# Performance work log

Hardware: AMD Instinct MI355X
Metric: run time of the kernel (lower is better)

## Reference

```python
import math
import jax, jax.numpy as jnp
import numpy as np

B, L, DIM, H = 2, 2048, 1024, 16
D = DIM // H  # head_dim = 64
EPS = 1e-6


def setup_inputs() -> dict:
    key = jax.random.key(0)
    ks = jax.random.split(key, 5)
    s = 0.02
    return {
        "x": jax.random.normal(ks[0], (B, L, DIM), jnp.float32),
        "pe": jax.random.normal(ks[1], (B, 1, L, D // 2, 2, 2), jnp.float32),
        "w_qkv": jax.random.normal(ks[2], (DIM, 3 * DIM), jnp.float32) * s,
        "q_scale": jnp.ones((D,), jnp.float32),
        "k_scale": jnp.ones((D,), jnp.float32),
        "w_proj": jax.random.normal(ks[3], (DIM, DIM), jnp.float32) * s,
        "b_proj": jnp.zeros((DIM,), jnp.float32),
    }


def _rmsnorm(t, scale):
    # flax nnx.RMSNorm: x * rsqrt(mean(x^2) + eps) * scale, over last dim
    var = jnp.mean(jnp.square(t), axis=-1, keepdims=True)
    return t * jax.lax.rsqrt(var + EPS) * scale


def _apply_rope(t, pe):
    # t: [B,H,L,D]; pe: [B,1,L,D/2,2,2]
    t2 = t.reshape(*t.shape[:-1], D // 2, 1, 2)
    out = pe[..., 0] * t2[..., 0] + pe[..., 1] * t2[..., 1]  # [B,H,L,D/2,2]
    return out.reshape(t.shape)


def reference(x, pe, w_qkv, q_scale, k_scale, w_proj, b_proj):
    # fused QKV projection
    qkv = jnp.einsum('bld,de->ble', x, w_qkv)  # [B,L,3*DIM]
    qkv = qkv.reshape(B, L, 3, H, D).transpose(2, 0, 3, 1, 4)  # [3,B,H,L,D]
    q, k, v = qkv[0], qkv[1], qkv[2]
    # QK RMSNorm
    q = _rmsnorm(q, q_scale)
    k = _rmsnorm(k, k_scale)
    # RoPE via pe
    q = _apply_rope(q, pe)
    k = _apply_rope(k, pe)
    # scaled dot product attention
    scores = jnp.einsum('bhqd,bhkd->bhqk', q, k) / math.sqrt(D)
    attn = jax.nn.softmax(scores, axis=-1)
    o = jnp.einsum('bhqk,bhkd->bhqd', attn, v)  # [B,H,L,D]
    o = o.transpose(0, 2, 1, 3).reshape(B, L, DIM)  # B H L D -> B L (H D)
    # output projection
    return jnp.einsum('bld,de->ble', o, w_proj) + b_proj
```

## Files before the change

### kernel.cpp

```cpp
#include <hip/hip_runtime.h>
#include <math.h>

#define BB 2
#define LL 2048
#define DIMM 1024
#define HH 16
#define DD 64
#define QKV_N 3072

typedef unsigned short u16;
typedef unsigned int u32;
typedef __attribute__((ext_vector_type(8))) short short8;
typedef __attribute__((ext_vector_type(4))) float f32x4;

__device__ __forceinline__ float bf2f(u16 h) {
    unsigned u = ((unsigned)h) << 16;
    return __uint_as_float(u);
}
__device__ __forceinline__ u16 f2bf(float f) {
    unsigned u = __float_as_uint(f);
    u += 0x7fffu + ((u >> 16) & 1u);
    return (u16)(u >> 16);
}
__device__ __forceinline__ u32 pack_bf2(float lo, float hi) {
    u32 a = __float_as_uint(hi) + 0x8000u;
    u32 b = __float_as_uint(lo) + 0x8000u;
    return __builtin_amdgcn_perm(a, b, 0x07060302u);
}
__device__ __forceinline__ void gload16(const u16* g, u16* l) {
    __builtin_amdgcn_global_load_lds(
        (const __attribute__((address_space(1))) void*)g,
        (__attribute__((address_space(3))) void*)l, 16, 0, 0);
}

__global__ __launch_bounds__(256) void convx(
    const float* __restrict__ X, u16* __restrict__ Xb)
{
    int i = (blockIdx.x * 256 + threadIdx.x) * 8;
    float4 a = *(const float4*)&X[i];
    float4 b = *(const float4*)&X[i + 4];
    u16 t[8] = {f2bf(a.x), f2bf(a.y), f2bf(a.z), f2bf(a.w),
                f2bf(b.x), f2bf(b.y), f2bf(b.z), f2bf(b.w)};
    *(uint4*)&Xb[i] = *(uint4*)t;
}

__global__ __launch_bounds__(256) void convt(
    const float* __restrict__ W, u16* __restrict__ Wt, int K, int N)
{
    __shared__ u16 s[64][72];
    const int tid = threadIdx.x;
    const int k0 = blockIdx.x * 64, n0 = blockIdx.y * 64;
#pragma unroll
    for (int t = 0; t < 16; ++t) {
        int flat = t * 256 + tid;
        int kk = flat >> 6, nn = flat & 63;
        s[nn][kk] = f2bf(W[(size_t)(k0 + kk) * N + n0 + nn]);
    }
    __syncthreads();
#pragma unroll
    for (int t = 0; t < 2; ++t) {
        int chunk = t * 256 + tid;
        int nn = chunk >> 3, kc = chunk & 7;
        *(uint4*)&Wt[(size_t)(n0 + nn) * K + k0 + kc * 8] = *(uint4*)&s[nn][kc * 8];
    }
}

__global__ __launch_bounds__(256) void gemm_qkv(
    const u16* __restrict__ A, const u16* __restrict__ Bt,
    u16* __restrict__ C, u16* __restrict__ vt, const float* __restrict__ pe,
    const float* __restrict__ qs, const float* __restrict__ ks)
{
    __shared__ u16 smem[2 * 128 * 64];
    u16* sA = smem;
    u16* sB = smem + 128 * 64;

    const int tid = threadIdx.x;
    const int wave = tid >> 6, lane = tid & 63;
    const int mIdx = lane & 15, quad = lane >> 4;
    const int wr = wave >> 1, wc = wave & 1;
    const int m0 = blockIdx.y * 128, n0 = blockIdx.x * 128;
    const int N = QKV_N, K = DIMM;
    const int lr = lane >> 3, lc = lane & 7;

    f32x4 acc[4][4];
#pragma unroll
    for (int a = 0; a < 4; ++a)
#pragma unroll
        for (int b = 0; b < 4; ++b) acc[a][b] = (f32x4){0.f, 0.f, 0.f, 0.f};

    for (int k0 = 0; k0 < K; k0 += 64) {
#pragma unroll
        for (int j = 0; j < 4; ++j) {
            int r0 = 32 * wave + 8 * j + lr;
            int kc = 8 * (lc ^ (r0 & 7));
            gload16(&A[(size_t)(m0 + r0) * K + k0 + kc], &sA[(32 * wave + 8 * j) * 64]);
            gload16(&Bt[(size_t)(n0 + r0) * K + k0 + kc], &sB[(32 * wave + 8 * j) * 64]);
        }
        __syncthreads();
#pragma unroll
        for (int ks2 = 0; ks2 < 2; ++ks2) {
            short8 af[4], bfr[4];
#pragma unroll
            for (int mt = 0; mt < 4; ++mt) {
                int Ra = 64 * wr + 16 * mt + mIdx;
                af[mt] = *(const short8*)&sA[Ra * 64 + 8 * ((ks2 * 4 + quad) ^ (Ra & 7))];
            }
#pragma unroll
            for (int nt = 0; nt < 4; ++nt) {
                int Rb = 64 * wc + 16 * nt + mIdx;
                bfr[nt] = *(const short8*)&sB[Rb * 64 + 8 * ((ks2 * 4 + quad) ^ (Rb & 7))];
            }
#pragma unroll
            for (int mt = 0; mt < 4; ++mt)
#pragma unroll
                for (int nt = 0; nt < 4; ++nt)
                    acc[mt][nt] = __builtin_amdgcn_mfma_f32_16x16x32_bf16(
                        af[mt], bfr[nt], acc[mt][nt], 0, 0, 0);
        }
        __syncthreads();
    }

    if (n0 >= 2048) {
#pragma unroll
        for (int mt = 0; mt < 4; ++mt) {
            int lofs = 64 * wr + 16 * mt + 4 * quad;
#pragma unroll
            for (int nt = 0; nt < 4; ++nt) {
                int d = 64 * wc + 16 * nt + mIdx;
                uint2 pr;
                pr.x = pack_bf2(acc[mt][nt][0], acc[mt][nt][1]);
                pr.y = pack_bf2(acc[mt][nt][2], acc[mt][nt][3]);
                *(uint2*)&smem[d * 128 + (lofs ^ (8 * (d & 7)))] = pr;
            }
        }
        __syncthreads();
        {
            const int d = tid >> 1, half = tid & 1;
            const int hd = n0 - 2048 + d;
            const int h = hd >> 6, dd = hd & 63;
            const int b = m0 >> 11, l0 = m0 & 2047;
            u16* dst = vt + ((size_t)((b * 16 + h) * 64 + dd)) * LL + l0 + half * 64;
#pragma unroll
            for (int c = 0; c < 8; ++c) {
                int slot = (half * 64 + 8 * c) ^ (8 * (d & 7));
                *(uint4*)&dst[8 * c] = *(const uint4*)&smem[d * 128 + slot];
            }
        }
    } else {
        const float* scv = (n0 < 1024) ? qs : ks;
        const float pre = (n0 < 1024) ? 0.18033688011112042f : 1.0f;
        float scl[4];
#pragma unroll
        for (int nt = 0; nt < 4; ++nt) scl[nt] = scv[16 * nt + mIdx];

#pragma unroll
        for (int mt = 0; mt < 4; ++mt) {
#pragma unroll
            for (int r = 0; r < 4; ++r) {
                float s = 0.f;
#pragma unroll
                for (int nt = 0; nt < 4; ++nt) {
                    float a = acc[mt][nt][r];
                    s += a * a;
                }
                s += __shfl_xor(s, 1);
                s += __shfl_xor(s, 2);
                s += __shfl_xor(s, 4);
                s += __shfl_xor(s, 8);
                float rn = rsqrtf(s * (1.f / 64.f) + 1e-6f);
                int R = m0 + 64 * wr + 16 * mt + quad * 4 + r;
                size_t peo = (size_t)R * 128;
#pragma unroll
                for (int nt = 0; nt < 4; ++nt) {
                    float v = acc[mt][nt][r] * rn * scl[nt];
                    float pp = __shfl_xor(v, 1);
                    float2 pw = *(const float2*)&pe[peo + 2 * (16 * nt + mIdx)];
                    float e  = (mIdx & 1) ? pp : v;
                    float od = (mIdx & 1) ? v : pp;
                    C[(size_t)R * N + n0 + 64 * wc + 16 * nt + mIdx] =
                        f2bf((pw.x * e + pw.y * od) * pre);
                }
            }
        }
    }
}

__global__ __launch_bounds__(256) void gemm_proj(
    const u16* __restrict__ A, const u16* __restrict__ Bt,
    const float* __restrict__ bias, float* __restrict__ C)
{
    __shared__ u16 sA[64 * 64];
    __shared__ u16 sB[128 * 64];

    const int tid = threadIdx.x;
    const int wave = tid >> 6, lane = tid & 63;
    const int mIdx = lane & 15, quad = lane >> 4;
    const int wr = wave >> 1, wc = wave & 1;
    const int m0 = blockIdx.y * 64, n0 = blockIdx.x * 128;
    const int N = DIMM, K = DIMM;
    const int lr = lane >> 3, lc = lane & 7;

    f32x4 acc[2][4];
#pragma unroll
    for (int a = 0; a < 2; ++a)
#pragma unroll
        for (int b = 0; b < 4; ++b) acc[a][b] = (f32x4){0.f, 0.f, 0.f, 0.f};

    for (int k0 = 0; k0 < K; k0 += 64) {
#pragma unroll
        for (int j = 0; j < 2; ++j) {
            int r0 = 16 * wave + 8 * j + lr;
            int kc = 8 * (lc ^ (r0 & 7));
            gload16(&A[(size_t)(m0 + r0) * K + k0 + kc], &sA[(16 * wave + 8 * j) * 64]);
        }
#pragma unroll
        for (int j = 0; j < 4; ++j) {
            int r0 = 32 * wave + 8 * j + lr;
            int kc = 8 * (lc ^ (r0 & 7));
            gload16(&Bt[(size_t)(n0 + r0) * K + k0 + kc], &sB[(32 * wave + 8 * j) * 64]);
        }
        __syncthreads();
#pragma unroll
        for (int ks2 = 0; ks2 < 2; ++ks2) {
            short8 af[2], bfr[4];
#pragma unroll
            for (int mt = 0; mt < 2; ++mt) {
                int Ra = 32 * wr + 16 * mt + mIdx;
                af[mt] = *(const short8*)&sA[Ra * 64 + 8 * ((ks2 * 4 + quad) ^ (Ra & 7))];
            }
#pragma unroll
            for (int nt = 0; nt < 4; ++nt) {
                int Rb = 64 * wc + 16 * nt + mIdx;
                bfr[nt] = *(const short8*)&sB[Rb * 64 + 8 * ((ks2 * 4 + quad) ^ (Rb & 7))];
            }
#pragma unroll
            for (int mt = 0; mt < 2; ++mt)
#pragma unroll
                for (int nt = 0; nt < 4; ++nt)
                    acc[mt][nt] = __builtin_amdgcn_mfma_f32_16x16x32_bf16(
                        af[mt], bfr[nt], acc[mt][nt], 0, 0, 0);
        }
        __syncthreads();
    }

#pragma unroll
    for (int mt = 0; mt < 2; ++mt)
#pragma unroll
        for (int r = 0; r < 4; ++r) {
            int row = m0 + 32 * wr + 16 * mt + quad * 4 + r;
#pragma unroll
            for (int nt = 0; nt < 4; ++nt) {
                int col = n0 + 64 * wc + 16 * nt + mIdx;
                C[(size_t)row * N + col] = acc[mt][nt][r] + bias[col];
            }
        }
}

__global__ __launch_bounds__(256, 2) void attn_mfma(
    const u16* __restrict__ qkv, const u16* __restrict__ vt, u16* __restrict__ o)
{
    __shared__ u16 sK[2][64 * 64];
    __shared__ u16 sVt[2][64 * 64];
    __shared__ u16 sP[128 * 64];

    const int tid = threadIdx.x;
    const int wave = tid >> 6;
    const int lane = tid & 63;
    const int mIdx = lane & 15;
    const int quad = lane >> 4;
    const int m7 = mIdx & 7;

    const int bh = blockIdx.x >> 4;
    const int qt = blockIdx.x & 15;
    const int b = bh >> 4, h = bh & 15;
    const int q0 = qt * 128;

    const u16* kbase = qkv + (size_t)b * LL * QKV_N + 1024 + h * 64;
    const u16* vbase = vt + (size_t)bh * 64 * LL;

    short8 aq[2][2];
#pragma unroll
    for (int g = 0; g < 2; ++g) {
        const u16* qrow = qkv + (size_t)b * LL * QKV_N + h * 64
                          + (size_t)(q0 + 32 * wave + 16 * g + mIdx) * QKV_N;
        aq[g][0] = *(const short8*)&qrow[quad * 8];
        aq[g][1] = *(const short8*)&qrow[32 + quad * 8];
    }

    const int lr = lane >> 3, lc = lane & 7;
    const int sw = 8 * (lc ^ lr);

#pragma unroll
    for (int i = 0; i < 2; ++i) {
        const int row = 16 * wave + 8 * i + lr;
        gload16(&kbase[(size_t)row * QKV_N + sw], &sK[0][(16 * wave + 8 * i) * 64]);
        gload16(&vbase[(size_t)row * LL + sw], &sVt[0][(16 * wave + 8 * i) * 64]);
    }

    float lsum[2] = {0.f, 0.f};
    f32x4 Oacc[2][4];
#pragma unroll
    for (int g = 0; g < 2; ++g)
#pragma unroll
        for (int nb = 0; nb < 4; ++nb) Oacc[g][nb] = (f32x4){0.f, 0.f, 0.f, 0.f};

    const int o0 = 8 * (quad ^ m7);
    const int o1 = 8 * ((quad + 4) ^ m7);
    u16* sPr0 = &sP[(32 * wave + mIdx) * 64];
    u16* sPr1 = &sP[(32 * wave + 16 + mIdx) * 64];

    for (int kt = 0; kt < 32; ++kt) {
        const int p = kt & 1;
        __syncthreads();

        if (kt + 1 < 32) {
            const int k0n = (kt + 1) * 64;
#pragma unroll
            for (int i = 0; i < 2; ++i) {
                const int row = 16 * wave + 8 * i + lr;
                gload16(&kbase[(size_t)(k0n + row) * QKV_N + sw],
                        &sK[p ^ 1][(16 * wave + 8 * i) * 64]);
                gload16(&vbase[(size_t)row * LL + k0n + sw],
                        &sVt[p ^ 1][(16 * wave + 8 * i) * 64]);
            }
        }

#pragma unroll
        for (int nb = 0; nb < 4; ++nb) {
            const u16* krow = &sK[p][(16 * nb + mIdx) * 64];
            short8 bk0 = *(const short8*)&krow[o0];
            short8 bk1 = *(const short8*)&krow[o1];
            const int pofs = (16 * nb + 4 * quad) ^ (8 * m7);
#pragma unroll
            for (int g = 0; g < 2; ++g) {
                f32x4 st = (f32x4){0.f, 0.f, 0.f, 0.f};
                st = __builtin_amdgcn_mfma_f32_16x16x32_bf16(bk0, aq[g][0], st, 0, 0, 0);
                st = __builtin_amdgcn_mfma_f32_16x16x32_bf16(bk1, aq[g][1], st, 0, 0, 0);
                float p0 = exp2f(st[0]), p1 = exp2f(st[1]);
                float p2 = exp2f(st[2]), p3 = exp2f(st[3]);
                lsum[g] += (p0 + p1) + (p2 + p3);
                uint2 wp;
                wp.x = pack_bf2(p0, p1);
                wp.y = pack_bf2(p2, p3);
                *(uint2*)&((g == 0 ? sPr0 : sPr1)[pofs]) = wp;
            }
        }

        short8 pa00 = *(const short8*)&sPr0[o0];
        short8 pa01 = *(const short8*)&sPr0[o1];
        short8 pa10 = *(const short8*)&sPr1[o0];
        short8 pa11 = *(const short8*)&sPr1[o1];
#pragma unroll
        for (int nb = 0; nb < 4; ++nb) {
            const u16* vrow = &sVt[p][(16 * nb + mIdx) * 64];
            short8 bv0 = *(const short8*)&vrow[o0];
            short8 bv1 = *(const short8*)&vrow[o1];
            Oacc[0][nb] = __builtin_amdgcn_mfma_f32_16x16x32_bf16(pa00, bv0, Oacc[0][nb], 0, 0, 0);
            Oacc[0][nb] = __builtin_amdgcn_mfma_f32_16x16x32_bf16(pa01, bv1, Oacc[0][nb], 0, 0, 0);
            Oacc[1][nb] = __builtin_amdgcn_mfma_f32_16x16x32_bf16(pa10, bv0, Oacc[1][nb], 0, 0, 0);
            Oacc[1][nb] = __builtin_amdgcn_mfma_f32_16x16x32_bf16(pa11, bv1, Oacc[1][nb], 0, 0, 0);
        }
    }

#pragma unroll
    for (int g = 0; g < 2; ++g) {
        float ls = lsum[g];
        ls += __shfl_xor(ls, 16);
        ls += __shfl_xor(ls, 32);
#pragma unroll
        for (int r = 0; r < 4; ++r) {
            float lv = __shfl(ls, quad * 4 + r);
            float linv = 1.f / lv;
            const int rowg = b * LL + q0 + 32 * wave + 16 * g + quad * 4 + r;
#pragma unroll
            for (int nb = 0; nb < 4; ++nb) {
                o[(size_t)rowg * DIMM + h * 64 + 16 * nb + mIdx] =
                    f2bf(Oacc[g][nb][r] * linv);
            }
        }
    }
}

extern "C" void kernel_launch(void* const* d_in, const int* in_sizes, int n_in,
                              void* d_out, int out_size, void* d_ws, size_t ws_size,
                              hipStream_t stream) {
    const float* x       = (const float*)d_in[0];
    const float* pe      = (const float*)d_in[1];
    const float* w_qkv   = (const float*)d_in[2];
    const float* q_scale = (const float*)d_in[3];
    const float* k_scale = (const float*)d_in[4];
    const float* w_proj  = (const float*)d_in[5];
    const float* b_proj  = (const float*)d_in[6];
    float* out = (float*)d_out;

    char* ws = (char*)d_ws;
    u16* qkv    = (u16*)ws;  ws += (size_t)4096 * 3072 * 2;
    u16* o      = (u16*)ws;  ws += (size_t)4096 * 1024 * 2;
    u16* xb     = (u16*)ws;  ws += (size_t)4096 * 1024 * 2;
    u16* wqkvt  = (u16*)ws;  ws += (size_t)3072 * 1024 * 2;
    u16* wprojt = (u16*)ws;  ws += (size_t)1024 * 1024 * 2;
    u16* vtbuf  = (u16*)ws;  ws += (size_t)BB * HH * DD * LL * 2;

    convx<<<(4096 * 1024) / (256 * 8), 256, 0, stream>>>(x, xb);
    convt<<<dim3(1024 / 64, QKV_N / 64), 256, 0, stream>>>(w_qkv, wqkvt, DIMM, QKV_N);
    convt<<<dim3(1024 / 64, 1024 / 64), 256, 0, stream>>>(w_proj, wprojt, DIMM, DIMM);

    gemm_qkv<<<dim3(QKV_N / 128, (BB * LL) / 128), 256, 0, stream>>>(
        xb, wqkvt, qkv, vtbuf, pe, q_scale, k_scale);

    attn_mfma<<<BB * HH * (LL / 128), 256, 0, stream>>>(qkv, vtbuf, o);

    gemm_proj<<<dim3(DIMM / 128, (BB * LL) / 64), 256, 0, stream>>>(
        o, wprojt, b_proj, out);
}
```

Baseline: 222.6 us.

## Pre-pack K/V into MFMA fragment layout and load directly to registers in attention

The QKV GEMM epilogue now writes K and V straight into a packed per-lane MFMA fragment layout, replacing the shared-memory transpose for V. The attention kernel loads K and V fragments directly from global memory into registers, double-buffering K across iterations, and drops the shared K/V tiles and their per-iteration barriers. The row sum is computed with MFMA against a ones vector instead of shuffles. Block IDs are remapped for locality and priority hints are set around the PV MFMAs. This removes LDS traffic and syncs but raises register pressure and relies on L2 for reuse across waves, since each wave now loads the same K/V independently.

Result: slower. 240.3 us (+7.9%).

```diff
diff --git a/kernel.cpp b/kernel.cpp
--- a/kernel.cpp
+++ b/kernel.cpp
@@ -67,7 +67,8 @@
 
 __global__ __launch_bounds__(256) void gemm_qkv(
     const u16* __restrict__ A, const u16* __restrict__ Bt,
-    u16* __restrict__ C, u16* __restrict__ vt, const float* __restrict__ pe,
+    u16* __restrict__ C, u16* __restrict__ kp, u16* __restrict__ vp,
+    const float* __restrict__ pe,
     const float* __restrict__ qs, const float* __restrict__ ks)
 {
     __shared__ u16 smem[2 * 128 * 64];
@@ -123,32 +124,27 @@
     if (n0 >= 2048) {
 #pragma unroll
         for (int mt = 0; mt < 4; ++mt) {
-            int lofs = 64 * wr + 16 * mt + 4 * quad;
+            const int R0 = m0 + 64 * wr + 16 * mt + 4 * quad;
+            const int bb = R0 >> 11;
+            const int t0 = R0 & 2047;
 #pragma unroll
             for (int nt = 0; nt < 4; ++nt) {
-                int d = 64 * wc + 16 * nt + mIdx;
+                const int hd = n0 - 2048 + 64 * wc + 16 * nt + mIdx;
+                const int h = hd >> 6, d = hd & 63;
+                const int bh = bb * 16 + h;
+                const size_t blk =
+                    ((size_t)(bh * 32 + (t0 >> 6)) * 4 + (d >> 4)) * 2 + ((t0 >> 5) & 1);
+                const int ln = (d & 15) + 16 * ((t0 >> 3) & 3);
                 uint2 pr;
                 pr.x = pack_bf2(acc[mt][nt][0], acc[mt][nt][1]);
                 pr.y = pack_bf2(acc[mt][nt][2], acc[mt][nt][3]);
-                *(uint2*)&smem[d * 128 + (lofs ^ (8 * (d & 7)))] = pr;
-            }
-        }
-        __syncthreads();
-        {
-            const int d = tid >> 1, half = tid & 1;
-            const int hd = n0 - 2048 + d;
-            const int h = hd >> 6, dd = hd & 63;
-            const int b = m0 >> 11, l0 = m0 & 2047;
-            u16* dst = vt + ((size_t)((b * 16 + h) * 64 + dd)) * LL + l0 + half * 64;
-#pragma unroll
-            for (int c = 0; c < 8; ++c) {
-                int slot = (half * 64 + 8 * c) ^ (8 * (d & 7));
-                *(uint4*)&dst[8 * c] = *(const uint4*)&smem[d * 128 + slot];
+                *(uint2*)&vp[blk * 512 + ln * 8 + (t0 & 7)] = pr;
             }
         }
     } else {
-        const float* scv = (n0 < 1024) ? qs : ks;
-        const float pre = (n0 < 1024) ? 0.18033688011112042f : 1.0f;
+        const bool isq = (n0 < 1024);
+        const float* scv = isq ? qs : ks;
+        const float pre = isq ? 0.18033688011112042f : 1.0f;
         float scl[4];
 #pragma unroll
         for (int nt = 0; nt < 4; ++nt) scl[nt] = scv[16 * nt + mIdx];
@@ -168,7 +164,8 @@
                 s += __shfl_xor(s, 4);
                 s += __shfl_xor(s, 8);
                 float rn = rsqrtf(s * (1.f / 64.f) + 1e-6f);
-                int R = m0 + 64 * wr + 16 * mt + quad * 4 + r;
+                const int R = m0 + 64 * wr + 16 * mt + quad * 4 + r;
+                const int bb = R >> 11, t = R & 2047;
                 size_t peo = (size_t)R * 128;
 #pragma unroll
                 for (int nt = 0; nt < 4; ++nt) {
@@ -177,8 +174,17 @@
                     float2 pw = *(const float2*)&pe[peo + 2 * (16 * nt + mIdx)];
                     float e  = (mIdx & 1) ? pp : v;
                     float od = (mIdx & 1) ? v : pp;
-                    C[(size_t)R * N + n0 + 64 * wc + 16 * nt + mIdx] =
-                        f2bf((pw.x * e + pw.y * od) * pre);
+                    u16 val = f2bf((pw.x * e + pw.y * od) * pre);
+                    if (isq) {
+                        C[(size_t)R * N + n0 + 64 * wc + 16 * nt + mIdx] = val;
+                    } else {
+                        const int col = n0 - 1024 + 64 * wc + 16 * nt + mIdx;
+                        const int h = col >> 6, d = col & 63;
+                        const size_t blk =
+                            ((size_t)((bb * 16 + h) * 32 + (t >> 6)) * 4 + ((t >> 4) & 3)) * 2
+                            + (d >> 5);
+                        kp[blk * 512 + ((t & 15) + 16 * ((d >> 3) & 3)) * 8 + (d & 7)] = val;
+                    }
                 }
             }
         }
@@ -257,10 +263,9 @@
 }
 
 __global__ __launch_bounds__(256, 2) void attn_mfma(
-    const u16* __restrict__ qkv, const u16* __restrict__ vt, u16* __restrict__ o)
+    const u16* __restrict__ qkv, const u16* __restrict__ kp,
+    const u16* __restrict__ vp, u16* __restrict__ o)
 {
-    __shared__ u16 sK[2][64 * 64];
-    __shared__ u16 sVt[2][64 * 64];
     __shared__ u16 sP[128 * 64];
 
     const int tid = threadIdx.x;
@@ -270,13 +275,14 @@
     const int quad = lane >> 4;
     const int m7 = mIdx & 7;
 
-    const int bh = blockIdx.x >> 4;
-    const int qt = blockIdx.x & 15;
+    const int bid = ((blockIdx.x & 7) << 6) | (blockIdx.x >> 3);
+    const int bh = bid >> 4;
+    const int qt = bid & 15;
     const int b = bh >> 4, h = bh & 15;
     const int q0 = qt * 128;
 
-    const u16* kbase = qkv + (size_t)b * LL * QKV_N + 1024 + h * 64;
-    const u16* vbase = vt + (size_t)bh * 64 * LL;
+    const u16* kbase = kp + (size_t)bh * 32 * 4096 + lane * 8;
+    const u16* vbase = vp + (size_t)bh * 32 * 4096 + lane * 8;
 
     short8 aq[2][2];
 #pragma unroll
@@ -287,90 +293,86 @@
         aq[g][1] = *(const short8*)&qrow[32 + quad * 8];
     }
 
-    const int lr = lane >> 3, lc = lane & 7;
-    const int sw = 8 * (lc ^ lr);
-
-#pragma unroll
-    for (int i = 0; i < 2; ++i) {
-        const int row = 16 * wave + 8 * i + lr;
-        gload16(&kbase[(size_t)row * QKV_N + sw], &sK[0][(16 * wave + 8 * i) * 64]);
-        gload16(&vbase[(size_t)row * LL + sw], &sVt[0][(16 * wave + 8 * i) * 64]);
-    }
-
-    float lsum[2] = {0.f, 0.f};
+    const short8 bones = {(short)0x3F80, (short)0x3F80, (short)0x3F80, (short)0x3F80,
+                          (short)0x3F80, (short)0x3F80, (short)0x3F80, (short)0x3F80};
+
+    float dummy;
     f32x4 Oacc[2][4];
-#pragma unroll
-    for (int g = 0; g < 2; ++g)
+    f32x4 lac[2];
+#pragma unroll
+    for (int g = 0; g < 2; ++g) {
+        lac[g] = (f32x4){0.f, 0.f, 0.f, 0.f};
 #pragma unroll
         for (int nb = 0; nb < 4; ++nb) Oacc[g][nb] = (f32x4){0.f, 0.f, 0.f, 0.f};
+    }
 
     const int o0 = 8 * (quad ^ m7);
     const int o1 = 8 * ((quad + 4) ^ m7);
     u16* sPr0 = &sP[(32 * wave + mIdx) * 64];
     u16* sPr1 = &sP[(32 * wave + 16 + mIdx) * 64];
 
-    for (int kt = 0; kt < 32; ++kt) {
-        const int p = kt & 1;
-        __syncthreads();
-
-        if (kt + 1 < 32) {
-            const int k0n = (kt + 1) * 64;
-#pragma unroll
-            for (int i = 0; i < 2; ++i) {
-                const int row = 16 * wave + 8 * i + lr;
-                gload16(&kbase[(size_t)(k0n + row) * QKV_N + sw],
-                        &sK[p ^ 1][(16 * wave + 8 * i) * 64]);
-                gload16(&vbase[(size_t)row * LL + k0n + sw],
-                        &sVt[p ^ 1][(16 * wave + 8 * i) * 64]);
-            }
-        }
+    short8 kfA[8], kfB[8], vf[8];
+
+#pragma unroll
+    for (int f = 0; f < 8; ++f) kfA[f] = *(const short8*)&kbase[f * 512];
+
+    auto body = [&](short8* KC, short8* KN, int kt) {
+        const size_t tb = (size_t)kt * 4096;
+#pragma unroll
+        for (int f = 0; f < 8; ++f) vf[f] = *(const short8*)&vbase[tb + f * 512];
+        if (kt < 31) {
+#pragma unroll
+            for (int f = 0; f < 8; ++f) KN[f] = *(const short8*)&kbase[tb + 4096 + f * 512];
+        }
+        __builtin_amdgcn_sched_barrier(0);
 
 #pragma unroll
         for (int nb = 0; nb < 4; ++nb) {
-            const u16* krow = &sK[p][(16 * nb + mIdx) * 64];
-            short8 bk0 = *(const short8*)&krow[o0];
-            short8 bk1 = *(const short8*)&krow[o1];
             const int pofs = (16 * nb + 4 * quad) ^ (8 * m7);
 #pragma unroll
             for (int g = 0; g < 2; ++g) {
                 f32x4 st = (f32x4){0.f, 0.f, 0.f, 0.f};
-                st = __builtin_amdgcn_mfma_f32_16x16x32_bf16(bk0, aq[g][0], st, 0, 0, 0);
-                st = __builtin_amdgcn_mfma_f32_16x16x32_bf16(bk1, aq[g][1], st, 0, 0, 0);
+                st = __builtin_amdgcn_mfma_f32_16x16x32_bf16(KC[nb * 2 + 0], aq[g][0], st, 0, 0, 0);
+                st = __builtin_amdgcn_mfma_f32_16x16x32_bf16(KC[nb * 2 + 1], aq[g][1], st, 0, 0, 0);
                 float p0 = exp2f(st[0]), p1 = exp2f(st[1]);
                 float p2 = exp2f(st[2]), p3 = exp2f(st[3]);
-                lsum[g] += (p0 + p1) + (p2 + p3);
                 uint2 wp;
                 wp.x = pack_bf2(p0, p1);
                 wp.y = pack_bf2(p2, p3);
                 *(uint2*)&((g == 0 ? sPr0 : sPr1)[pofs]) = wp;
             }
         }
-
         short8 pa00 = *(const short8*)&sPr0[o0];
         short8 pa01 = *(const short8*)&sPr0[o1];
         short8 pa10 = *(const short8*)&sPr1[o0];
         short8 pa11 = *(const short8*)&sPr1[o1];
+
+        lac[0] = __builtin_amdgcn_mfma_f32_16x16x32_bf16(pa00, bones, lac[0], 0, 0, 0);
+        lac[0] = __builtin_amdgcn_mfma_f32_16x16x32_bf16(pa01, bones, lac[0], 0, 0, 0);
+        lac[1] = __builtin_amdgcn_mfma_f32_16x16x32_bf16(pa10, bones, lac[1], 0, 0, 0);
+        lac[1] = __builtin_amdgcn_mfma_f32_16x16x32_bf16(pa11, bones, lac[1], 0, 0, 0);
+
+        __builtin_amdgcn_s_setprio(1);
 #pragma unroll
         for (int nb = 0; nb < 4; ++nb) {
-            const u16* vrow = &sVt[p][(16 * nb + mIdx) * 64];
-            short8 bv0 = *(const short8*)&vrow[o0];
-            short8 bv1 = *(const short8*)&vrow[o1];
-            Oacc[0][nb] = __builtin_amdgcn_mfma_f32_16x16x32_bf16(pa00, bv0, Oacc[0][nb], 0, 0, 0);
-            Oacc[0][nb] = __builtin_amdgcn_mfma_f32_16x16x32_bf16(pa01, bv1, Oacc[0][nb], 0, 0, 0);
-            Oacc[1][nb] = __builtin_amdgcn_mfma_f32_16x16x32_bf16(pa10, bv0, Oacc[1][nb], 0, 0, 0);
-            Oacc[1][nb] = __builtin_amdgcn_mfma_f32_16x16x32_bf16(pa11, bv1, Oacc[1][nb], 0, 0, 0);
-        }
-    }
-
-#pragma unroll
-    for (int g = 0; g < 2; ++g) {
-        float ls = lsum[g];
-        ls += __shfl_xor(ls, 16);
-        ls += __shfl_xor(ls, 32);
+            Oacc[0][nb] = __builtin_amdgcn_mfma_f32_16x16x32_bf16(pa00, vf[nb * 2 + 0], Oacc[0][nb], 0, 0, 0);
+            Oacc[0][nb] = __builtin_amdgcn_mfma_f32_16x16x32_bf16(pa01, vf[nb * 2 + 1], Oacc[0][nb], 0, 0, 0);
+            Oacc[1][nb] = __builtin_amdgcn_mfma_f32_16x16x32_bf16(pa10, vf[nb * 2 + 0], Oacc[1][nb], 0, 0, 0);
+            Oacc[1][nb] = __builtin_amdgcn_mfma_f32_16x16x32_bf16(pa11, vf[nb * 2 + 1], Oacc[1][nb], 0, 0, 0);
+        }
+        __builtin_amdgcn_s_setprio(0);
+    };
+
+    for (int kt2 = 0; kt2 < 16; ++kt2) {
+        body(kfA, kfB, 2 * kt2);
+        body(kfB, kfA, 2 * kt2 + 1);
+    }
+
+#pragma unroll
+    for (int g = 0; g < 2; ++g)
 #pragma unroll
         for (int r = 0; r < 4; ++r) {
-            float lv = __shfl(ls, quad * 4 + r);
-            float linv = 1.f / lv;
+            float linv = 1.f / lac[g][r];
             const int rowg = b * LL + q0 + 32 * wave + 16 * g + quad * 4 + r;
 #pragma unroll
             for (int nb = 0; nb < 4; ++nb) {
@@ -378,7 +380,6 @@
                     f2bf(Oacc[g][nb][r] * linv);
             }
         }
-    }
 }
 
 extern "C" void kernel_launch(void* const* d_in, const int* in_sizes, int n_in,
@@ -399,16 +400,17 @@
     u16* xb     = (u16*)ws;  ws += (size_t)4096 * 1024 * 2;
     u16* wqkvt  = (u16*)ws;  ws += (size_t)3072 * 1024 * 2;
     u16* wprojt = (u16*)ws;  ws += (size_t)1024 * 1024 * 2;
-    u16* vtbuf  = (u16*)ws;  ws += (size_t)BB * HH * DD * LL * 2;
+    u16* kpack  = (u16*)ws;  ws += (size_t)32 * 32 * 4096 * 2;
+    u16* vpack  = (u16*)ws;  ws += (size_t)32 * 32 * 4096 * 2;
 
     convx<<<(4096 * 1024) / (256 * 8), 256, 0, stream>>>(x, xb);
     convt<<<dim3(1024 / 64, QKV_N / 64), 256, 0, stream>>>(w_qkv, wqkvt, DIMM, QKV_N);
     convt<<<dim3(1024 / 64, 1024 / 64), 256, 0, stream>>>(w_proj, wprojt, DIMM, DIMM);
 
     gemm_qkv<<<dim3(QKV_N / 128, (BB * LL) / 128), 256, 0, stream>>>(
-        xb, wqkvt, qkv, vtbuf, pe, q_scale, k_scale);
-
-    attn_mfma<<<BB * HH * (LL / 128), 256, 0, stream>>>(qkv, vtbuf, o);
+        xb, wqkvt, qkv, kpack, vpack, pe, q_scale, k_scale);
+
+    attn_mfma<<<BB * HH * (LL / 128), 256, 0, stream>>>(qkv, kpack, vpack, o);
 
     gemm_proj<<<dim3(DIMM / 128, (BB * LL) / 64), 256, 0, stream>>>(
         o, wprojt, b_proj, out);
```
